# Kernel tuning notes

Measured on AMD Instinct MI355X. Metric: run time of the kernel, lower is better.

The kernel has to match this reference:

```python
import jax, jax.numpy as jnp
import numpy as np

WIN = (8, 8)        # window height, width
HEADS = 6
DIM = 192
HEAD_DIM = DIM // HEADS
SCALE = HEAD_DIM ** -0.5
ALPHA = 0.2         # leaky_relu negative slope (tf.nn.leaky_relu / keras default)


def _leaky(t):
    return jnp.where(t >= 0, t, ALPHA * t)


def _relative_position_index():
    # Faithful to the TF code: tf.meshgrid defaults to 'xy' indexing.
    wh, ww = WIN
    mh, mw = jnp.meshgrid(jnp.arange(wh), jnp.arange(ww))  # each [ww, wh] (xy)
    coords = jnp.stack([mh, mw])                           # [2, ww, wh]
    flat = coords.reshape(2, -1)                           # [2, N]
    rel = flat[:, :, None] - flat[:, None, :]              # [2, N, N]
    rel = jnp.transpose(rel, (1, 2, 0))                    # [N, N, 2]
    idx = (rel[:, :, 0] + wh - 1) * (2 * ww - 1) + (rel[:, :, 1] + ww - 1)
    return idx                                             # [N, N] int32


def setup_inputs() -> dict:
    key = jax.random.key(0)
    ks = jax.random.split(key, 6)
    B_, N, C = 4096, WIN[0] * WIN[1], DIM
    std = 0.02
    return {
        "x": jax.random.normal(ks[0], (B_, N, C), dtype=jnp.float32),
        "wq": jax.random.normal(ks[1], (C, C), dtype=jnp.float32) * (C ** -0.5),
        "bq": jnp.zeros((C,), dtype=jnp.float32),
        "wkv": jax.random.normal(ks[2], (C, 2 * C), dtype=jnp.float32) * (C ** -0.5),
        "bkv": jnp.zeros((2 * C,), dtype=jnp.float32),
        "bias_table": jax.random.normal(ks[3], ((2 * WIN[0] - 1) * (2 * WIN[1] - 1), HEADS), dtype=jnp.float32) * std,
        "proj_w": jax.random.normal(ks[4], (C, C), dtype=jnp.float32) * (C ** -0.5),
        "proj_b": jnp.zeros((C,), dtype=jnp.float32),
    }


def reference(x, wq, bq, wkv, bkv, bias_table, proj_w, proj_b):
    B_, N, C = x.shape
    H, D = HEADS, HEAD_DIM

    # QKV projections with LeakyReLU activation (as in LinearProjection)
    q = _leaky(x @ wq + bq).reshape(B_, N, H, D).transpose(0, 2, 1, 3)      # [B,H,N,D]
    kv = _leaky(x @ wkv + bkv).reshape(B_, N, 2, H, D).transpose(2, 0, 3, 1, 4)
    k, v = kv[0], kv[1]                                                      # [B,H,N,D]

    # scaled attention scores
    attn = jnp.einsum('bhnd,bhmd->bhnm', q * SCALE, k)                       # [B,H,N,N]

    # gathered relative position bias (ratio == 1 here, tf.repeat is no-op)
    idx = _relative_position_index()                                         # [N,N]
    bias = bias_table[idx]                                                   # [N,N,H]
    attn = attn + jnp.transpose(bias, (2, 0, 1))[None]                       # [B,H,N,N]

    attn = jax.nn.softmax(attn, axis=-1)
    out = jnp.einsum('bhnm,bhmd->bhnd', attn, v)                             # [B,H,N,D]
    out = out.transpose(0, 2, 1, 3).reshape(B_, N, C)
    return out @ proj_w + proj_b
```

## Files before the change

kernel.cpp:

```cpp
#include <hip/hip_runtime.h>
#include <hip/hip_bf16.h>

typedef __bf16 bf16;
typedef bf16 bf16x8 __attribute__((ext_vector_type(8)));
typedef bf16 bf16x4 __attribute__((ext_vector_type(4)));
typedef short s16x4 __attribute__((ext_vector_type(4)));
typedef float f32x4 __attribute__((ext_vector_type(4)));

#define SCALE 0.17677669529663687f

#define XSTR 208
#define FSTR 196
#define OFF_F 13312
#define SMEM_ELEMS 38400

#if defined(__has_builtin)
#if __has_builtin(__builtin_amdgcn_mfma_f32_16x16x16bf16_1k)
#define HAS_MFMA16 1
#endif
#endif

__global__ void wattn_prep(const float* __restrict__ wq, const float* __restrict__ wkv,
                           const float* __restrict__ bias_table, const float* __restrict__ proj_w,
                           bf16* __restrict__ wqkvT, bf16* __restrict__ projT,
                           float* __restrict__ biasB)
{
    int t = blockIdx.x * 256 + threadIdx.x;
    if (t < 110592) {
        int n = t / 192, k = t % 192;
        float v = (n < 192) ? wq[k * 192 + n] : wkv[k * 384 + (n - 192)];
        wqkvT[t] = (bf16)v;
    } else if (t < 147456) {
        int e = t - 110592;
        int n = e / 192, k = e % 192;
        projT[e] = (bf16)proj_w[k * 192 + n];
    } else if (t < 172032) {
        int e = t - 147456;
        int h  = e >> 12;
        int mb = (e >> 8) & 15;
        int n  = (e >> 2) & 63;
        int mr = e & 3;
        int m  = mb * 4 + mr;
        int idx = ((n & 7) - (m & 7) + 7) * 15 + ((n >> 3) - (m >> 3) + 7);
        biasB[e] = bias_table[idx * 6 + h];
    }
}

#if !defined(HAS_MFMA16)
__device__ __forceinline__ bf16x8 build8(bf16x4 t0, bf16x4 t1, int li, int gi) {
    union { bf16x4 v; unsigned u[2]; } a0, a1;
    a0.v = t0; a1.v = t1;
    int b = li + 32 * (gi & 1);
    unsigned l0  = __shfl(a0.u[0], b),      l1  = __shfl(a0.u[1], b);
    unsigned l0h = __shfl(a0.u[0], b + 16), l1h = __shfl(a0.u[1], b + 16);
    unsigned h0  = __shfl(a1.u[0], b),      h1  = __shfl(a1.u[1], b);
    unsigned h0h = __shfl(a1.u[0], b + 16), h1h = __shfl(a1.u[1], b + 16);
    bool hi = (gi & 2);
    union { bf16x8 v8; unsigned u[4]; } r;
    r.u[0] = hi ? h0 : l0;   r.u[1] = hi ? h1 : l1;
    r.u[2] = hi ? h0h : l0h; r.u[3] = hi ? h1h : l1h;
    return r.v8;
}
#endif

__global__ __launch_bounds__(384, 4)
void wattn_main(const float* __restrict__ x, const bf16* __restrict__ wqkvT,
                const float* __restrict__ bq, const float* __restrict__ bkv,
                const bf16* __restrict__ projT, const float* __restrict__ biasB,
                const float* __restrict__ proj_b, float* __restrict__ outg)
{
    __shared__ __align__(16) bf16 smem[SMEM_ELEMS];
    const int tid = threadIdx.x;
    const int li  = tid & 15;
    const int gi  = (tid >> 4) & 3;
    const int w   = tid >> 6;
    const int win = blockIdx.x;

    bf16* xb = smem;
    const int srow = tid / 48, scol = tid % 48;
    const f32x4 fz = {0.f, 0.f, 0.f, 0.f};

    {
        const float4* xg = (const float4*)(x + (size_t)win * 12288);
#pragma unroll
        for (int i = 0; i < 8; ++i) {
            float4 p = xg[(srow + 8 * i) * 48 + scol];
            bf16x4 v; v[0]=(bf16)p.x; v[1]=(bf16)p.y; v[2]=(bf16)p.z; v[3]=(bf16)p.w;
            *(bf16x4*)&xb[(srow + 8 * i) * XSTR + scol * 4] = v;
        }
    }
    __syncthreads();

    bf16x4 qf[2][4], kf[2][4];
    {
        f32x4 aqk[4][4];
#pragma unroll
        for (int j = 0; j < 4; ++j)
#pragma unroll
            for (int c = 0; c < 4; ++c) aqk[j][c] = fz;
#pragma unroll 2
        for (int kk = 0; kk < 6; ++kk) {
            bf16x8 bx[4], aw[4];
#pragma unroll
            for (int c = 0; c < 4; ++c)
                bx[c] = *(const bf16x8*)&xb[(c * 16 + li) * XSTR + kk * 32 + gi * 8];
#pragma unroll
            for (int j = 0; j < 4; ++j) {
                int T = (j < 2) ? (2 * w + j) : (12 + 2 * w + (j - 2));
                aw[j] = *(const bf16x8*)&wqkvT[(size_t)(T * 16 + li) * 192 + kk * 32 + gi * 8];
            }
#pragma unroll
            for (int j = 0; j < 4; ++j)
#pragma unroll
                for (int c = 0; c < 4; ++c)
                    aqk[j][c] = __builtin_amdgcn_mfma_f32_16x16x32_bf16(aw[j], bx[c], aqk[j][c], 0, 0, 0);
        }
#pragma unroll
        for (int j = 0; j < 2; ++j) {
            f32x4 bjq = *(const f32x4*)&bq [32 * w + 16 * j + 4 * gi];
            f32x4 bjk = *(const f32x4*)&bkv[32 * w + 16 * j + 4 * gi];
#pragma unroll
            for (int c = 0; c < 4; ++c) {
                bf16x4 rq, rk;
#pragma unroll
                for (int rg = 0; rg < 4; ++rg) {
                    float tq = aqk[j][c][rg]     + bjq[rg];
                    float tk = aqk[2 + j][c][rg] + bjk[rg];
                    tq = (fmaxf(tq, 0.f) + 0.2f * fminf(tq, 0.f)) * SCALE;
                    tk =  fmaxf(tk, 0.f) + 0.2f * fminf(tk, 0.f);
                    rq[rg] = (bf16)tq;
                    rk[rg] = (bf16)tk;
                }
                qf[j][c] = rq;
                kf[j][c] = rk;
            }
        }
    }

    f32x4 s[4][4];
#if defined(HAS_MFMA16)
#pragma unroll
    for (int cm = 0; cm < 4; ++cm)
#pragma unroll
        for (int cn = 0; cn < 4; ++cn) {
            f32x4 t = __builtin_amdgcn_mfma_f32_16x16x16bf16_1k(
                __builtin_bit_cast(s16x4, kf[0][cm]), __builtin_bit_cast(s16x4, qf[0][cn]), fz, 0, 0, 0);
            s[cm][cn] = __builtin_amdgcn_mfma_f32_16x16x16bf16_1k(
                __builtin_bit_cast(s16x4, kf[1][cm]), __builtin_bit_cast(s16x4, qf[1][cn]), t, 0, 0, 0);
        }
#else
    {
        bf16x8 ka[4], qb[4];
#pragma unroll
        for (int cm = 0; cm < 4; ++cm) ka[cm] = build8(kf[0][cm], kf[1][cm], li, gi);
#pragma unroll
        for (int cn = 0; cn < 4; ++cn) qb[cn] = build8(qf[0][cn], qf[1][cn], li, gi);
#pragma unroll
        for (int cm = 0; cm < 4; ++cm)
#pragma unroll
            for (int cn = 0; cn < 4; ++cn)
                s[cm][cn] = __builtin_amdgcn_mfma_f32_16x16x32_bf16(ka[cm], qb[cn], fz, 0, 0, 0);
    }
#endif

    float rs[4];
    bf16x4 pb[4][4];
#pragma unroll
    for (int cn = 0; cn < 4; ++cn) {
        float m_ = -1e30f;
#pragma unroll
        for (int cm = 0; cm < 4; ++cm) {
            s[cm][cn] += *(const f32x4*)&biasB[w * 4096 + (4 * cm + gi) * 256 + (16 * cn + li) * 4];
#pragma unroll
            for (int rg = 0; rg < 4; ++rg) m_ = fmaxf(m_, s[cm][cn][rg]);
        }
        m_ = fmaxf(m_, __shfl_xor(m_, 16));
        m_ = fmaxf(m_, __shfl_xor(m_, 32));
        float ss = 0.f;
#pragma unroll
        for (int cm = 0; cm < 4; ++cm) {
            bf16x4 r;
#pragma unroll
            for (int rg = 0; rg < 4; ++rg) {
                float p = __expf(s[cm][cn][rg] - m_);
                ss += p;
                r[rg] = (bf16)p;
            }
            pb[cm][cn] = r;
        }
        ss += __shfl_xor(ss, 16);
        ss += __shfl_xor(ss, 32);
        rs[cn] = 1.f / ss;
    }

    bf16x4 vf[2][4];
    {
        f32x4 av_[4][2];
#pragma unroll
        for (int rt = 0; rt < 4; ++rt)
#pragma unroll
            for (int j = 0; j < 2; ++j) av_[rt][j] = fz;
#pragma unroll 2
        for (int kk = 0; kk < 6; ++kk) {
            bf16x8 a[4], bwv[2];
#pragma unroll
            for (int rt = 0; rt < 4; ++rt)
                a[rt] = *(const bf16x8*)&xb[(rt * 16 + li) * XSTR + kk * 32 + gi * 8];
#pragma unroll
            for (int j = 0; j < 2; ++j)
                bwv[j] = *(const bf16x8*)&wqkvT[(size_t)((24 + 2 * w + j) * 16 + li) * 192 + kk * 32 + gi * 8];
#pragma unroll
            for (int rt = 0; rt < 4; ++rt)
#pragma unroll
                for (int j = 0; j < 2; ++j)
                    av_[rt][j] = __builtin_amdgcn_mfma_f32_16x16x32_bf16(a[rt], bwv[j], av_[rt][j], 0, 0, 0);
        }
#pragma unroll
        for (int j = 0; j < 2; ++j) {
            f32x4 bjv = *(const f32x4*)&bkv[192 + 32 * w + 16 * j + 4 * gi];
#pragma unroll
            for (int rt = 0; rt < 4; ++rt) {
                bf16x4 r;
#pragma unroll
                for (int rg = 0; rg < 4; ++rg) {
                    float t = av_[rt][j][rg] + bjv[rg];
                    t = fmaxf(t, 0.f) + 0.2f * fminf(t, 0.f);
                    r[rg] = (bf16)t;
                }
                vf[j][rt] = r;
            }
        }
    }

    f32x4 o[2][4];
#pragma unroll
    for (int ct = 0; ct < 2; ++ct)
#pragma unroll
        for (int cn = 0; cn < 4; ++cn) {
#if defined(HAS_MFMA16)
            f32x4 t = fz;
#pragma unroll
            for (int rt = 0; rt < 4; ++rt)
                t = __builtin_amdgcn_mfma_f32_16x16x16bf16_1k(
                        __builtin_bit_cast(s16x4, vf[ct][rt]),
                        __builtin_bit_cast(s16x4, pb[rt][cn]), t, 0, 0, 0);
            o[ct][cn] = t;
#else
            f32x4 t = fz;
#pragma unroll
            for (int c = 0; c < 2; ++c)
                t = __builtin_amdgcn_mfma_f32_16x16x32_bf16(
                        build8(vf[ct][2 * c], vf[ct][2 * c + 1], li, gi),
                        build8(pb[2 * c][cn], pb[2 * c + 1][cn], li, gi), t, 0, 0, 0);
            o[ct][cn] = t;
#endif
        }
    __syncthreads();

#pragma unroll
    for (int ct = 0; ct < 2; ++ct)
#pragma unroll
        for (int cn = 0; cn < 4; ++cn) {
            bf16x4 r;
#pragma unroll
            for (int rg = 0; rg < 4; ++rg) r[rg] = (bf16)(o[ct][cn][rg] * rs[cn]);
            *(bf16x4*)&xb[(cn * 16 + li) * XSTR + 32 * w + 16 * ct + 4 * gi] = r;
        }
    __syncthreads();

    f32x4 pa[2][4];
#pragma unroll
    for (int ct = 0; ct < 2; ++ct)
#pragma unroll
        for (int cn = 0; cn < 4; ++cn) pa[ct][cn] = fz;
#pragma unroll 2
    for (int kk = 0; kk < 6; ++kk) {
        bf16x8 bo[4], awp[2];
#pragma unroll
        for (int cn = 0; cn < 4; ++cn)
            bo[cn] = *(const bf16x8*)&xb[(cn * 16 + li) * XSTR + kk * 32 + gi * 8];
#pragma unroll
        for (int ct = 0; ct < 2; ++ct)
            awp[ct] = *(const bf16x8*)&projT[(size_t)((2 * w + ct) * 16 + li) * 192 + kk * 32 + gi * 8];
#pragma unroll
        for (int ct = 0; ct < 2; ++ct)
#pragma unroll
            for (int cn = 0; cn < 4; ++cn)
                pa[ct][cn] = __builtin_amdgcn_mfma_f32_16x16x32_bf16(awp[ct], bo[cn], pa[ct][cn], 0, 0, 0);
    }

    {
        float* of = (float*)(smem + OFF_F);
#pragma unroll
        for (int ct = 0; ct < 2; ++ct) {
            f32x4 pbv = *(const f32x4*)&proj_b[32 * w + 16 * ct + 4 * gi];
#pragma unroll
            for (int cn = 0; cn < 4; ++cn) {
                f32x4 y = pa[ct][cn];
#pragma unroll
                for (int rg = 0; rg < 4; ++rg) y[rg] += pbv[rg];
                *(f32x4*)&of[(cn * 16 + li) * FSTR + 32 * w + 16 * ct + 4 * gi] = y;
            }
        }
    }
    __syncthreads();

    {
        const float* of = (const float*)(smem + OFF_F);
        float4* og = (float4*)(outg + (size_t)win * 12288);
#pragma unroll
        for (int i = 0; i < 8; ++i)
            og[(srow + 8 * i) * 48 + scol] = *(const float4*)&of[(srow + 8 * i) * FSTR + scol * 4];
    }
}

extern "C" void kernel_launch(void* const* d_in, const int* in_sizes, int n_in,
                              void* d_out, int out_size, void* d_ws, size_t ws_size,
                              hipStream_t stream)
{
    const float* x          = (const float*)d_in[0];
    const float* wq         = (const float*)d_in[1];
    const float* bq         = (const float*)d_in[2];
    const float* wkv        = (const float*)d_in[3];
    const float* bkv        = (const float*)d_in[4];
    const float* bias_table = (const float*)d_in[5];
    const float* proj_w     = (const float*)d_in[6];
    const float* proj_b     = (const float*)d_in[7];
    float* out = (float*)d_out;

    int B = in_sizes[0] / (64 * 192);

    bf16*  wqkvT = (bf16*)d_ws;
    bf16*  projT = (bf16*)((char*)d_ws + 221184);
    float* biasB = (float*)((char*)d_ws + 294912);

    wattn_prep<<<672, 256, 0, stream>>>(wq, wkv, bias_table, proj_w, wqkvT, projT, biasB);

    wattn_main<<<B, 384, 0, stream>>>(x, wqkvT, bq, bkv, projT, biasB, proj_b, out);
}
```

Measured before the change: 265.1 us.

## Fold biases into MFMA accumulators and write output via shuffles instead of LDS

Bias vectors for Q/K/V, the relative-position bias, and the projection bias now initialize the MFMA accumulators rather than being added afterwards. The final output is no longer staged through an fp32 LDS buffer with an extra barrier. Lanes exchange values with __shfl and store float4s straight to global memory. This cuts shared memory from about 77KB to about 27KB per block, which should raise occupancy, at the cost of extra cross-lane shuffles and possibly less coalesced global stores.

```diff
diff --git a/kernel.cpp b/kernel.cpp
--- a/kernel.cpp
+++ b/kernel.cpp
@@ -10,9 +10,7 @@
 #define SCALE 0.17677669529663687f
 
 #define XSTR 208
-#define FSTR 196
-#define OFF_F 13312
-#define SMEM_ELEMS 38400
+#define SMEM_ELEMS 13312
 
 #if defined(__has_builtin)
 #if __has_builtin(__builtin_amdgcn_mfma_f32_16x16x16bf16_1k)
@@ -93,11 +91,16 @@
 
     bf16x4 qf[2][4], kf[2][4];
     {
+        f32x4 bjq0 = *(const f32x4*)&bq [32 * w + 4 * gi];
+        f32x4 bjq1 = *(const f32x4*)&bq [32 * w + 16 + 4 * gi];
+        f32x4 bjk0 = *(const f32x4*)&bkv[32 * w + 4 * gi];
+        f32x4 bjk1 = *(const f32x4*)&bkv[32 * w + 16 + 4 * gi];
         f32x4 aqk[4][4];
 #pragma unroll
-        for (int j = 0; j < 4; ++j)
-#pragma unroll
-            for (int c = 0; c < 4; ++c) aqk[j][c] = fz;
+        for (int c = 0; c < 4; ++c) {
+            aqk[0][c] = bjq0; aqk[1][c] = bjq1;
+            aqk[2][c] = bjk0; aqk[3][c] = bjk1;
+        }
 #pragma unroll 2
         for (int kk = 0; kk < 6; ++kk) {
             bf16x8 bx[4], aw[4];
@@ -116,16 +119,14 @@
                     aqk[j][c] = __builtin_amdgcn_mfma_f32_16x16x32_bf16(aw[j], bx[c], aqk[j][c], 0, 0, 0);
         }
 #pragma unroll
-        for (int j = 0; j < 2; ++j) {
-            f32x4 bjq = *(const f32x4*)&bq [32 * w + 16 * j + 4 * gi];
-            f32x4 bjk = *(const f32x4*)&bkv[32 * w + 16 * j + 4 * gi];
+        for (int j = 0; j < 2; ++j)
 #pragma unroll
             for (int c = 0; c < 4; ++c) {
                 bf16x4 rq, rk;
 #pragma unroll
                 for (int rg = 0; rg < 4; ++rg) {
-                    float tq = aqk[j][c][rg]     + bjq[rg];
-                    float tk = aqk[2 + j][c][rg] + bjk[rg];
+                    float tq = aqk[j][c][rg];
+                    float tk = aqk[2 + j][c][rg];
                     tq = (fmaxf(tq, 0.f) + 0.2f * fminf(tq, 0.f)) * SCALE;
                     tk =  fmaxf(tk, 0.f) + 0.2f * fminf(tk, 0.f);
                     rq[rg] = (bf16)tq;
@@ -134,34 +135,24 @@
                 qf[j][c] = rq;
                 kf[j][c] = rk;
             }
-        }
     }
 
     f32x4 s[4][4];
+#pragma unroll
+    for (int cm = 0; cm < 4; ++cm)
+#pragma unroll
+        for (int cn = 0; cn < 4; ++cn) {
+            f32x4 bv = *(const f32x4*)&biasB[w * 4096 + (4 * cm + gi) * 256 + (16 * cn + li) * 4];
 #if defined(HAS_MFMA16)
-#pragma unroll
-    for (int cm = 0; cm < 4; ++cm)
-#pragma unroll
-        for (int cn = 0; cn < 4; ++cn) {
             f32x4 t = __builtin_amdgcn_mfma_f32_16x16x16bf16_1k(
-                __builtin_bit_cast(s16x4, kf[0][cm]), __builtin_bit_cast(s16x4, qf[0][cn]), fz, 0, 0, 0);
+                __builtin_bit_cast(s16x4, kf[0][cm]), __builtin_bit_cast(s16x4, qf[0][cn]), bv, 0, 0, 0);
             s[cm][cn] = __builtin_amdgcn_mfma_f32_16x16x16bf16_1k(
                 __builtin_bit_cast(s16x4, kf[1][cm]), __builtin_bit_cast(s16x4, qf[1][cn]), t, 0, 0, 0);
-        }
 #else
-    {
-        bf16x8 ka[4], qb[4];
-#pragma unroll
-        for (int cm = 0; cm < 4; ++cm) ka[cm] = build8(kf[0][cm], kf[1][cm], li, gi);
-#pragma unroll
-        for (int cn = 0; cn < 4; ++cn) qb[cn] = build8(qf[0][cn], qf[1][cn], li, gi);
-#pragma unroll
-        for (int cm = 0; cm < 4; ++cm)
-#pragma unroll
-            for (int cn = 0; cn < 4; ++cn)
-                s[cm][cn] = __builtin_amdgcn_mfma_f32_16x16x32_bf16(ka[cm], qb[cn], fz, 0, 0, 0);
-    }
-#endif
+            s[cm][cn] = __builtin_amdgcn_mfma_f32_16x16x32_bf16(
+                build8(kf[0][cm], kf[1][cm], li, gi), build8(qf[0][cn], qf[1][cn], li, gi), bv, 0, 0, 0);
+#endif
+        }
 
     float rs[4];
     bf16x4 pb[4][4];
@@ -169,11 +160,9 @@
     for (int cn = 0; cn < 4; ++cn) {
         float m_ = -1e30f;
 #pragma unroll
-        for (int cm = 0; cm < 4; ++cm) {
-            s[cm][cn] += *(const f32x4*)&biasB[w * 4096 + (4 * cm + gi) * 256 + (16 * cn + li) * 4];
+        for (int cm = 0; cm < 4; ++cm)
 #pragma unroll
             for (int rg = 0; rg < 4; ++rg) m_ = fmaxf(m_, s[cm][cn][rg]);
-        }
         m_ = fmaxf(m_, __shfl_xor(m_, 16));
         m_ = fmaxf(m_, __shfl_xor(m_, 32));
         float ss = 0.f;
@@ -195,11 +184,11 @@
 
     bf16x4 vf[2][4];
     {
+        f32x4 bjv0 = *(const f32x4*)&bkv[192 + 32 * w + 4 * gi];
+        f32x4 bjv1 = *(const f32x4*)&bkv[192 + 32 * w + 16 + 4 * gi];
         f32x4 av_[4][2];
 #pragma unroll
-        for (int rt = 0; rt < 4; ++rt)
-#pragma unroll
-            for (int j = 0; j < 2; ++j) av_[rt][j] = fz;
+        for (int rt = 0; rt < 4; ++rt) { av_[rt][0] = bjv0; av_[rt][1] = bjv1; }
 #pragma unroll 2
         for (int kk = 0; kk < 6; ++kk) {
             bf16x8 a[4], bwv[2];
@@ -216,20 +205,18 @@
                     av_[rt][j] = __builtin_amdgcn_mfma_f32_16x16x32_bf16(a[rt], bwv[j], av_[rt][j], 0, 0, 0);
         }
 #pragma unroll
-        for (int j = 0; j < 2; ++j) {
-            f32x4 bjv = *(const f32x4*)&bkv[192 + 32 * w + 16 * j + 4 * gi];
+        for (int j = 0; j < 2; ++j)
 #pragma unroll
             for (int rt = 0; rt < 4; ++rt) {
                 bf16x4 r;
 #pragma unroll
                 for (int rg = 0; rg < 4; ++rg) {
-                    float t = av_[rt][j][rg] + bjv[rg];
+                    float t = av_[rt][j][rg];
                     t = fmaxf(t, 0.f) + 0.2f * fminf(t, 0.f);
                     r[rg] = (bf16)t;
                 }
                 vf[j][rt] = r;
             }
-        }
     }
 
     f32x4 o[2][4];
@@ -269,10 +256,12 @@
     __syncthreads();
 
     f32x4 pa[2][4];
-#pragma unroll
-    for (int ct = 0; ct < 2; ++ct)
-#pragma unroll
-        for (int cn = 0; cn < 4; ++cn) pa[ct][cn] = fz;
+    {
+        f32x4 pb0 = *(const f32x4*)&proj_b[32 * w + 4 * gi];
+        f32x4 pb1 = *(const f32x4*)&proj_b[32 * w + 16 + 4 * gi];
+#pragma unroll
+        for (int cn = 0; cn < 4; ++cn) { pa[0][cn] = pb0; pa[1][cn] = pb1; }
+    }
 #pragma unroll 2
     for (int kk = 0; kk < 6; ++kk) {
         bf16x8 bo[4], awp[2];
@@ -290,27 +279,19 @@
     }
 
     {
-        float* of = (float*)(smem + OFF_F);
-#pragma unroll
-        for (int ct = 0; ct < 2; ++ct) {
-            f32x4 pbv = *(const f32x4*)&proj_b[32 * w + 16 * ct + 4 * gi];
-#pragma unroll
-            for (int cn = 0; cn < 4; ++cn) {
-                f32x4 y = pa[ct][cn];
-#pragma unroll
-                for (int rg = 0; rg < 4; ++rg) y[rg] += pbv[rg];
-                *(f32x4*)&of[(cn * 16 + li) * FSTR + 32 * w + 16 * ct + 4 * gi] = y;
-            }
-        }
-    }
-    __syncthreads();
-
-    {
-        const float* of = (const float*)(smem + OFF_F);
-        float4* og = (float4*)(outg + (size_t)win * 12288);
-#pragma unroll
-        for (int i = 0; i < 8; ++i)
-            og[(srow + 8 * i) * 48 + scol] = *(const float4*)&of[(srow + 8 * i) * FSTR + scol * 4];
+        const int L = tid & 63;
+        const int src = (L >> 2) + 16 * (L & 3);
+        f32x4* og = (f32x4*)(outg + (size_t)win * 12288);
+#pragma unroll
+        for (int cn = 0; cn < 4; ++cn)
+#pragma unroll
+            for (int ct = 0; ct < 2; ++ct) {
+                f32x4 y;
+#pragma unroll
+                for (int e = 0; e < 4; ++e)
+                    y[e] = __shfl(pa[ct][cn][e], src);
+                og[(16 * cn + (L >> 2)) * 48 + 8 * w + 4 * ct + (L & 3)] = y;
+            }
     }
 }
 
```

After: 241.8 us. -8.8%, faster.
